# Optimization experiments

Measured on AMD Instinct MI355X. Metric: run time of the kernel, lower is better.

Reference implementation:

```python
import jax, jax.numpy as jnp
import numpy as np

B, S, E, H = 4, 2048, 256, 8
DK = E // H


def setup_inputs() -> dict:
    key = jax.random.key(0)
    ks = jax.random.split(key, 12)
    glorot = lambda k, shape: jax.random.uniform(k, shape, jnp.float32, -1.0, 1.0) * jnp.sqrt(6.0 / (shape[0] + shape[1]))
    inp = {
        "q": jax.random.normal(ks[0], (B, S, E), jnp.float32),
        "k": jax.random.normal(ks[1], (B, S, E), jnp.float32),
        "v": jax.random.normal(ks[2], (B, S, E), jnp.float32),
        # causal mask, np.triu(k=1)==0 -> lower triangular including diagonal
        "mask": (jnp.triu(jnp.ones((S, S), jnp.int32), k=1) == 0).astype(jnp.int32)[None, None],
        "Wq": glorot(ks[3], (E, E)), "bq": jnp.zeros((E,), jnp.float32),
        "Wk": glorot(ks[4], (E, E)), "bk": jnp.zeros((E,), jnp.float32),
        "Wv": glorot(ks[5], (E, E)), "bv": jnp.zeros((E,), jnp.float32),
        "Wo": glorot(ks[6], (E, E)), "bo": jnp.zeros((E,), jnp.float32),
        "gammas": glorot(ks[7], (H, 1)).reshape(H, 1, 1),  # xavier init of (H,1,1)
    }
    return inp


def reference(q, k, v, mask, Wq, bq, Wk, bk, Wv, bv, Wo, bo, gammas):
    b, s, e = q.shape
    h = gammas.shape[0]
    dk = e // h
    neg = jnp.float32(-1e32)

    def proj(x, W, bias):
        return (x @ W.T + bias).reshape(b, s, h, dk).transpose(0, 2, 1, 3)  # [B,H,S,dk]

    qh, kh, vh = proj(q, Wq, bq), proj(k, Wk, bk), proj(v, Wv, bv)
    scores = jnp.einsum("bhid,bhjd->bhij", qh, kh) / jnp.sqrt(jnp.float32(dk))  # [B,H,S,S]

    # --- no_grad block: monotonic distance-decay term ---
    maskf = mask.astype(scores.dtype)
    s1 = jax.nn.softmax(jnp.where(mask == 0, neg, scores), axis=-1) * maskf
    s1 = jax.lax.stop_gradient(s1)
    distcum = jnp.cumsum(s1, axis=-1)
    disttotal = jnp.sum(s1, axis=-1, keepdims=True)
    idx = jnp.arange(s)
    pos = jnp.abs(idx[None, :] - idx[:, None]).astype(scores.dtype)[None, None]  # |i-j|
    dist = jnp.sqrt(jnp.clip((disttotal - distcum) * pos, 0.0, None))
    dist = jax.lax.stop_gradient(dist)
    # ----------------------------------------------------

    gamma = -jax.nn.softplus(gammas)[None]                      # [1,H,1,1]
    total_effect = jnp.clip(jnp.exp(dist * gamma), 1e-5, 1e5)
    scores = jnp.where(mask == 0, neg, scores * total_effect)
    attn = jax.nn.softmax(scores, axis=-1)                      # zero_pad=False (mask=1 path)
    out = jnp.einsum("bhij,bhjd->bhid", attn, vh)
    concat = out.transpose(0, 2, 1, 3).reshape(b, s, e)
    return concat @ Wo.T + bo
```

## Files before the change

kernel.cpp:

```cpp
#include <hip/hip_runtime.h>
#include <math.h>

#define B_   4
#define S_   2048
#define E_   256
#define H_   8
#define DK_  32
#define NROWS (B_*S_)

typedef unsigned short ushort_t;
typedef __attribute__((ext_vector_type(8))) short  bf16x8;
typedef __attribute__((ext_vector_type(4))) float  f32x4;

#define LOG2E 1.4426950408889634f
#define QSCALE (0.17677669529663687f * 1.4426950408889634f)

#if __has_builtin(__builtin_amdgcn_exp2f)
#define EXP2F(x) __builtin_amdgcn_exp2f(x)
#else
#define EXP2F(x) exp2f(x)
#endif
#if __has_builtin(__builtin_amdgcn_sqrtf)
#define SQRTF(x) __builtin_amdgcn_sqrtf(x)
#else
#define SQRTF(x) sqrtf(x)
#endif
#if __has_builtin(__builtin_amdgcn_rcpf)
#define RCPF(x) __builtin_amdgcn_rcpf(x)
#else
#define RCPF(x) (1.0f/(x))
#endif

__device__ __forceinline__ ushort_t bf16_rne(float x)
{
    unsigned int u = __float_as_uint(x);
    unsigned int r = u + 0x7FFFu + ((u >> 16) & 1u);
    return (ushort_t)(r >> 16);
}
__device__ __forceinline__ float bf16_to_f(ushort_t h)
{
    return __uint_as_float(((unsigned int)h) << 16);
}

__device__ __forceinline__ float scan16(float x)
{
    x += __int_as_float(__builtin_amdgcn_update_dpp(0, __float_as_int(x), 0x111, 0xF, 0xF, true));
    x += __int_as_float(__builtin_amdgcn_update_dpp(0, __float_as_int(x), 0x112, 0xF, 0xF, true));
    x += __int_as_float(__builtin_amdgcn_update_dpp(0, __float_as_int(x), 0x114, 0xF, 0xF, true));
    x += __int_as_float(__builtin_amdgcn_update_dpp(0, __float_as_int(x), 0x118, 0xF, 0xF, true));
    return x;
}
__device__ __forceinline__ float bcast15(float x)
{
    return __int_as_float(__builtin_amdgcn_ds_swizzle(__float_as_int(x), 0x1F0));
}


__global__ __launch_bounds__(256)
void conv_w(const float* __restrict__ Wq, const float* __restrict__ Wk,
            const float* __restrict__ Wv, const float* __restrict__ Wo,
            ushort_t* __restrict__ wh, ushort_t* __restrict__ wl)
{
    const int z = blockIdx.y;
    const float* src = (z == 0) ? Wq : (z == 1) ? Wk : (z == 2) ? Wv : Wo;
    ushort_t* dh = wh + (size_t)z * (E_ * E_);
    ushort_t* dl = wl + (size_t)z * (E_ * E_);
    const int n0 = blockIdx.x * 16;
    const int lr = threadIdx.x & 15, kq = threadIdx.x >> 4;
    #pragma unroll
    for (int half = 0; half < 2; half++) {
        const int kk = kq * 8 + half * 128;
        const float* s = src + (size_t)(n0 + lr) * E_ + kk;
        const float4 a = *(const float4*)s;
        const float4 b = *(const float4*)(s + 4);
        const float xs[8] = {a.x, a.y, a.z, a.w, b.x, b.y, b.z, b.w};
        bf16x8 hv, lv;
        #pragma unroll
        for (int e = 0; e < 8; e++) {
            const ushort_t hb = bf16_rne(xs[e]);
            hv[e] = (short)hb;
            lv[e] = (short)bf16_rne(xs[e] - bf16_to_f(hb));
        }
        const size_t o = ((size_t)blockIdx.x * 8 + (kk >> 5)) * 512
                       + ((kk >> 3) & 3) * 128 + lr * 8;
        *(bf16x8*)&dh[o] = hv;
        *(bf16x8*)&dl[o] = lv;
    }
}

__global__ __launch_bounds__(256)
void gemm_qkv(const float* __restrict__ Xq, const float* __restrict__ Xk,
              const float* __restrict__ Xv,
              const ushort_t* __restrict__ Wh, const ushort_t* __restrict__ Wl,
              const float* __restrict__ bqp, const float* __restrict__ bkp,
              const float* __restrict__ bvp,
              ushort_t* __restrict__ Qh, ushort_t* __restrict__ Ql,
              ushort_t* __restrict__ Kh, ushort_t* __restrict__ Kl,
              ushort_t* __restrict__ Vt)
{
    __shared__ __align__(16) float sF[4][16][68];
    ushort_t* sBh = (ushort_t*)&sF[0][0][0];
    ushort_t* sBl = sBh + 4096;

    const size_t WN = (size_t)E_ * E_;
    const int z = blockIdx.z;
    const float* Xf = (z == 0) ? Xq : (z == 1) ? Xk : Xv;
    const ushort_t* Bh = Wh + (size_t)z * WN;
    const ushort_t* Bl = Wl + (size_t)z * WN;
    const float* bias = (z == 0) ? bqp : (z == 1) ? bkp : bvp;
    const float scale = (z == 0) ? QSCALE : 1.0f;

    const int lane = threadIdx.x & 63, wv = threadIdx.x >> 6;
    const int lr = lane & 15, lq = lane >> 4;
    const int mb = blockIdx.x;
    const int nstrip = blockIdx.y * 4 + wv;

    const float* arow = Xf + (size_t)(nstrip * 16 + lr) * E_ + lq * 8;
    const size_t boff = (size_t)(mb * 4 + wv) * 8 * 512 + lane * 8;
    const int lw = wv * 512 + lane * 8;

    f32x4 acc[4] = {{0,0,0,0},{0,0,0,0},{0,0,0,0},{0,0,0,0}};

    float4 a0 = *(const float4*)(arow);
    float4 a1 = *(const float4*)(arow + 4);
    {
        const bf16x8 sH = *(const bf16x8*)(Bh + boff);
        const bf16x8 sL = *(const bf16x8*)(Bl + boff);
        *(bf16x8*)&sBh[lw] = sH;
        *(bf16x8*)&sBl[lw] = sL;
    }

    #pragma unroll
    for (int kc = 0; kc < 8; kc++) {
        __syncthreads();
        const int cur = (kc & 1) * 2048;
        float4 a0n, a1n; bf16x8 sH2, sL2;
        if (kc < 7) {
            a0n = *(const float4*)(arow + (kc + 1) * 32);
            a1n = *(const float4*)(arow + (kc + 1) * 32 + 4);
            sH2 = *(const bf16x8*)(Bh + boff + (size_t)(kc + 1) * 512);
            sL2 = *(const bf16x8*)(Bl + boff + (size_t)(kc + 1) * 512);
        }
        bf16x8 aH, aL;
        {
            const float xs[8] = {a0.x, a0.y, a0.z, a0.w, a1.x, a1.y, a1.z, a1.w};
            #pragma unroll
            for (int e = 0; e < 8; e++) {
                const ushort_t hb = bf16_rne(xs[e]);
                aH[e] = (short)hb;
                aL[e] = (short)bf16_rne(xs[e] - bf16_to_f(hb));
            }
        }
        #pragma unroll
        for (int t = 0; t < 4; t++) {
            const int ro = cur + t * 512 + lane * 8;
            const bf16x8 bH = *(const bf16x8*)&sBh[ro];
            const bf16x8 bL = *(const bf16x8*)&sBl[ro];
            acc[t] = __builtin_amdgcn_mfma_f32_16x16x32_bf16(aL, bH, acc[t], 0, 0, 0);
            acc[t] = __builtin_amdgcn_mfma_f32_16x16x32_bf16(aH, bL, acc[t], 0, 0, 0);
            acc[t] = __builtin_amdgcn_mfma_f32_16x16x32_bf16(aH, bH, acc[t], 0, 0, 0);
        }
        if (kc < 7) {
            const int nx = (cur ^ 2048) + lw;
            *(bf16x8*)&sBh[nx] = sH2;
            *(bf16x8*)&sBl[nx] = sL2;
            a0 = a0n; a1 = a1n;
        }
    }
    __syncthreads();

    if (z <= 1) {
        #pragma unroll
        for (int t = 0; t < 4; t++) {
            const float bt = bias[mb * 64 + t * 16 + lr];
            #pragma unroll
            for (int reg = 0; reg < 4; reg++)
                sF[wv][lq * 4 + reg][t * 16 + lr] = (acc[t][reg] + bt) * scale;
        }
        ushort_t* Y1 = z ? Kh : Qh;
        ushort_t* Y2 = z ? Kl : Ql;
        const int bI   = nstrip >> 7;
        const int sblk = nstrip & 127;
        const int qg = lane >> 4, s = lane & 15;
        #pragma unroll
        for (int cg = 0; cg < 2; cg++) {
            const float* src = &sF[wv][s][cg * 32 + qg * 8];
            const float4 v0 = *(const float4*)src;
            const float4 v1 = *(const float4*)(src + 4);
            const float xs[8] = {v0.x, v0.y, v0.z, v0.w, v1.x, v1.y, v1.z, v1.w};
            bf16x8 hv, lv;
            #pragma unroll
            for (int e = 0; e < 8; e++) {
                const ushort_t hb = bf16_rne(xs[e]);
                hv[e] = (short)hb;
                lv[e] = (short)bf16_rne(xs[e] - bf16_to_f(hb));
            }
            const int h = mb * 2 + cg;
            const size_t o = (size_t)(bI * H_ + h) * (S_ * DK_)
                           + (size_t)sblk * 512 + lane * 8;
            *(bf16x8*)&Y1[o] = hv;
            *(bf16x8*)&Y2[o] = lv;
        }
    } else {
        #pragma unroll
        for (int t = 0; t < 4; t++) {
            const int col = mb * 64 + t * 16 + lr;
            const float bt = bias[col];
            const int h = col >> 5, d = col & 31;
            #pragma unroll
            for (int reg = 0; reg < 4; reg++) {
                const int n  = nstrip * 16 + lq * 4 + reg;
                const int bI = n >> 11, sI = n & (S_ - 1);
                const size_t o = (size_t)(bI * H_ + h) * (S_ * DK_)
                               + (size_t)((sI >> 5) * 2 + (d >> 4)) * 512
                               + ((sI >> 3) & 3) * 128 + (d & 15) * 8 + (sI & 7);
                Vt[o] = bf16_rne(acc[t][reg] + bt);
            }
        }
    }
}

__global__ __launch_bounds__(256)
void gemm_out(const ushort_t* __restrict__ Xh, const ushort_t* __restrict__ Xl,
              const ushort_t* __restrict__ Wh, const ushort_t* __restrict__ Wl,
              const float* __restrict__ bias, float* __restrict__ Yf)
{
    __shared__ __align__(16) ushort_t sBh[2 * 2048];
    __shared__ __align__(16) ushort_t sBl[2 * 2048];

    const int lane = threadIdx.x & 63, wv = threadIdx.x >> 6;
    const int lr = lane & 15, lq = lane >> 4;
    const int mb = blockIdx.x;
    const int nstrip = blockIdx.y * 4 + wv;

    const size_t aoff = (size_t)nstrip * 8 * 512 + lane * 8;
    const size_t boff = (size_t)(mb * 4 + wv) * 8 * 512 + lane * 8;
    const int lw = wv * 512 + lane * 8;

    f32x4 acc[4] = {{0,0,0,0},{0,0,0,0},{0,0,0,0},{0,0,0,0}};

    bf16x8 aH = *(const bf16x8*)(Xh + aoff);
    bf16x8 aL = *(const bf16x8*)(Xl + aoff);
    {
        const bf16x8 sH = *(const bf16x8*)(Wh + boff);
        const bf16x8 sL = *(const bf16x8*)(Wl + boff);
        *(bf16x8*)&sBh[lw] = sH;
        *(bf16x8*)&sBl[lw] = sL;
    }

    #pragma unroll
    for (int kc = 0; kc < 8; kc++) {
        __syncthreads();
        const int cur = (kc & 1) * 2048;
        bf16x8 aH2, aL2, sH2, sL2;
        if (kc < 7) {
            aH2 = *(const bf16x8*)(Xh + aoff + (size_t)(kc + 1) * 512);
            aL2 = *(const bf16x8*)(Xl + aoff + (size_t)(kc + 1) * 512);
            sH2 = *(const bf16x8*)(Wh + boff + (size_t)(kc + 1) * 512);
            sL2 = *(const bf16x8*)(Wl + boff + (size_t)(kc + 1) * 512);
        }
        #pragma unroll
        for (int t = 0; t < 4; t++) {
            const int ro = cur + t * 512 + lane * 8;
            const bf16x8 bH = *(const bf16x8*)&sBh[ro];
            const bf16x8 bL = *(const bf16x8*)&sBl[ro];
            acc[t] = __builtin_amdgcn_mfma_f32_16x16x32_bf16(aL, bH, acc[t], 0, 0, 0);
            acc[t] = __builtin_amdgcn_mfma_f32_16x16x32_bf16(aH, bL, acc[t], 0, 0, 0);
            acc[t] = __builtin_amdgcn_mfma_f32_16x16x32_bf16(aH, bH, acc[t], 0, 0, 0);
        }
        if (kc < 7) {
            const int nx = (cur ^ 2048) + lw;
            *(bf16x8*)&sBh[nx] = sH2;
            *(bf16x8*)&sBl[nx] = sL2;
            aH = aH2; aL = aL2;
        }
    }

    #pragma unroll
    for (int t = 0; t < 4; t++) {
        const int col = mb * 64 + t * 16 + lr;
        const float bt = bias[col];
        #pragma unroll
        for (int reg = 0; reg < 4; reg++) {
            const int n = nstrip * 16 + lq * 4 + reg;
            Yf[(size_t)n * E_ + col] = acc[t][reg] + bt;
        }
    }
}

#define VPAD 72

__device__ __forceinline__ void score_tile(f32x4 (&a)[4],
    const ushort_t* __restrict__ Kbh, const ushort_t* __restrict__ Kbl,
    int jt, const bf16x8& qhi, const bf16x8& qlo, int lane, int lr, int lq,
    bool domask, int i0)
{
    #pragma unroll
    for (int tt = 0; tt < 4; tt++) {
        const size_t ko = (size_t)(jt * 4 + tt) * 512 + lane * 8;
        const bf16x8 khi = *(const bf16x8*)(Kbh + ko);
        const bf16x8 klo = *(const bf16x8*)(Kbl + ko);
        f32x4 v = {0.f, 0.f, 0.f, 0.f};
        v = __builtin_amdgcn_mfma_f32_16x16x32_bf16(qlo, khi, v, 0, 0, 0);
        v = __builtin_amdgcn_mfma_f32_16x16x32_bf16(qhi, klo, v, 0, 0, 0);
        v = __builtin_amdgcn_mfma_f32_16x16x32_bf16(qhi, khi, v, 0, 0, 0);
        a[tt] = v;
    }
    if (domask) {
        #pragma unroll
        for (int tt = 0; tt < 4; tt++)
            #pragma unroll
            for (int r = 0; r < 4; r++) {
                const int irow = i0 + lq * 4 + r;
                const int j    = jt * 64 + tt * 16 + lr;
                if (j > irow) a[tt][r] = -3.0e38f;
            }
    }
}

__global__ __launch_bounds__(256)
void attn_flash(const ushort_t* __restrict__ Qh, const ushort_t* __restrict__ Ql,
                const ushort_t* __restrict__ Kh, const ushort_t* __restrict__ Kl,
                const ushort_t* __restrict__ Vs, const float* __restrict__ gammas,
                ushort_t* __restrict__ Ch, ushort_t* __restrict__ Cl)
{
    __shared__ float sTS[16][36];
    __shared__ __align__(16) ushort_t sP[4][16 * VPAD];
    __shared__ float sO[4][16][32];
    __shared__ float sZ[4][16];

    const int tid  = threadIdx.x;
    const int lane = tid & 63, wv = tid >> 6;
    const int lr   = lane & 15, lq = lane >> 4;
    const int bh   = blockIdx.x & 31;
    const int st   = (blockIdx.x >> 5) & 3;
    const int tq   = 31 - (blockIdx.x >> 7);
    const int h    = bh & 7, b = bh >> 3;
    const int i0   = tq * 64 + st * 16;

    const size_t hb = (size_t)bh * (S_ * DK_);
    const ushort_t* Kbh = Kh + hb;
    const ushort_t* Kbl = Kl + hb;
    const ushort_t* Vb  = Vs + hb;

    const float g   = gammas[h];
    const float gl2 = -((g > 20.f) ? g : log1pf(__expf(g))) * LOG2E;

    const size_t qoff = hb + (size_t)(i0 >> 4) * 512 + lane * 8;
    const bf16x8 qhi = *(const bf16x8*)(Qh + qoff);
    const bf16x8 qlo = *(const bf16x8*)(Ql + qoff);

    for (int jt = wv; jt <= tq; jt += 4) {
        f32x4 a[4];
        score_tile(a, Kbh, Kbl, jt, qhi, qlo, lane, lr, lq, jt == tq, i0);
        #pragma unroll
        for (int r = 0; r < 4; r++) {
            float rs = (EXP2F(a[0][r]) + EXP2F(a[1][r]))
                     + (EXP2F(a[2][r]) + EXP2F(a[3][r]));
            rs += __shfl_xor(rs, 1); rs += __shfl_xor(rs, 2);
            rs += __shfl_xor(rs, 4); rs += __shfl_xor(rs, 8);
            if (lr == 0) sTS[lq * 4 + r][jt] = rs;
        }
    }
    __syncthreads();

    float z2a[4] = {0.f, 0.f, 0.f, 0.f};
    f32x4 O0 = {0.f,0.f,0.f,0.f}, O1 = {0.f,0.f,0.f,0.f};

    if (wv <= tq) {
        float invZ[4], base[4], pr[4];
        #pragma unroll
        for (int r = 0; r < 4; r++) {
            const int row = lq * 4 + r;
            float run = 0.f, bs = 0.f;
            for (int t = 0; t <= tq; t++) {
                if (t < wv) bs += sTS[row][t];
                run += sTS[row][t];
            }
            invZ[r] = RCPF(run);
            base[r] = bs;
            pr[r]   = (float)(i0 + row - lr);
        }

        ushort_t* sPw = &sP[wv][0];
        for (int jt = wv; jt <= tq; jt += 4) {
            const int j0 = jt * 64;
            f32x4 a[4];
            score_tile(a, Kbh, Kbl, jt, qhi, qlo, lane, lr, lq, jt == tq, i0);

            float sc[4][4], tot[4][4];
            #pragma unroll
            for (int tt = 0; tt < 4; tt++)
                #pragma unroll
                for (int r = 0; r < 4; r++) {
                    const float e = EXP2F(a[tt][r]);
                    const float s = scan16(e);
                    sc[tt][r]  = s;
                    tot[tt][r] = bcast15(s);
                }
            #pragma unroll
            for (int r = 0; r < 4; r++) {
                float run2 = base[r];
                #pragma unroll
                for (int tt = 0; tt < 4; tt++) { sc[tt][r] += run2; run2 += tot[tt][r]; }
            }
            #pragma unroll
            for (int tt = 0; tt < 4; tt++) {
                const float jf = (float)(j0 + tt * 16);
                #pragma unroll
                for (int r = 0; r < 4; r++) {
                    const float rest = fmaf(-sc[tt][r], invZ[r], 1.0f);
                    const float posf = pr[r] - jf;
                    const float dist = SQRTF(fmaxf(rest * posf, 0.f));
                    const float eff  = EXP2F(gl2 * dist);
                    const float p2   = EXP2F(a[tt][r] * eff);
                    z2a[r] += p2;
                    sPw[(lq * 4 + r) * VPAD + tt * 16 + lr] = bf16_rne(p2);
                }
            }
            #pragma unroll
            for (int kc = 0; kc < 2; kc++) {
                const bf16x8 pa = *(const bf16x8*)&sPw[lr * VPAD + kc * 32 + lq * 8];
                const size_t vb = (size_t)(((j0 >> 5) + kc) * 2) * 512 + lane * 8;
                const bf16x8 v0 = *(const bf16x8*)(Vb + vb);
                const bf16x8 v1 = *(const bf16x8*)(Vb + vb + 512);
                O0 = __builtin_amdgcn_mfma_f32_16x16x32_bf16(pa, v0, O0, 0, 0, 0);
                O1 = __builtin_amdgcn_mfma_f32_16x16x32_bf16(pa, v1, O1, 0, 0, 0);
            }
            if (jt + 4 <= tq) {
                #pragma unroll
                for (int r = 0; r < 4; r++) {
                    const int row = lq * 4 + r;
                    base[r] += sTS[row][jt] + sTS[row][jt+1] + sTS[row][jt+2] + sTS[row][jt+3];
                }
            }
        }
    }

    #pragma unroll
    for (int r = 0; r < 4; r++) {
        float z = z2a[r];
        z += __shfl_xor(z, 1); z += __shfl_xor(z, 2);
        z += __shfl_xor(z, 4); z += __shfl_xor(z, 8);
        if (lr == 0) sZ[wv][lq * 4 + r] = z;
        sO[wv][lq * 4 + r][lr]      = O0[r];
        sO[wv][lq * 4 + r][16 + lr] = O1[r];
    }
    __syncthreads();

    #pragma unroll
    for (int p = 0; p < 2; p++) {
        const int pid = tid + p * 256;
        const int row = pid >> 5, d = pid & 31;
        const float v = (sO[0][row][d] + sO[1][row][d]) + (sO[2][row][d] + sO[3][row][d]);
        const float z = (sZ[0][row] + sZ[1][row]) + (sZ[2][row] + sZ[3][row]);
        const float y = v * RCPF(z);
        const int nIdx = b * S_ + i0 + row;
        const size_t o = ((size_t)(nIdx >> 4) * 8 + h) * 512
                       + (d >> 3) * 128 + (nIdx & 15) * 8 + (d & 7);
        const ushort_t hbb = bf16_rne(y);
        Ch[o] = hbb;
        Cl[o] = bf16_rne(y - bf16_to_f(hbb));
    }
}

extern "C" void kernel_launch(void* const* d_in, const int* in_sizes, int n_in,
                              void* d_out, int out_size, void* d_ws, size_t ws_size,
                              hipStream_t stream)
{
    const float* q      = (const float*)d_in[0];
    const float* k      = (const float*)d_in[1];
    const float* v      = (const float*)d_in[2];
    const float* Wq     = (const float*)d_in[4];
    const float* bq     = (const float*)d_in[5];
    const float* Wk     = (const float*)d_in[6];
    const float* bk     = (const float*)d_in[7];
    const float* Wv     = (const float*)d_in[8];
    const float* bv     = (const float*)d_in[9];
    const float* Wo     = (const float*)d_in[10];
    const float* bo     = (const float*)d_in[11];
    const float* gammas = (const float*)d_in[12];
    float* out = (float*)d_out;

    const size_t N2 = (size_t)NROWS * E_;
    const size_t WN = (size_t)E_ * E_;

    ushort_t* wh = (ushort_t*)d_ws;
    ushort_t* wl = wh + 4 * WN;
    ushort_t* qh = wl + 4 * WN;
    ushort_t* ql = qh + N2;
    ushort_t* kh = ql + N2;
    ushort_t* kl = kh + N2;
    ushort_t* vt = kl + N2;
    ushort_t* ch = vt + N2;
    ushort_t* cl = ch + N2;

    conv_w<<<dim3(16, 4), 256, 0, stream>>>(Wq, Wk, Wv, Wo, wh, wl);

    gemm_qkv<<<dim3(E_ / 64, NROWS / 64, 3), 256, 0, stream>>>(
        q, k, v, wh, wl, bq, bk, bv, qh, ql, kh, kl, vt);

    attn_flash<<<32 * 32 * 4, 256, 0, stream>>>(qh, ql, kh, kl, vt, gammas, ch, cl);

    gemm_out<<<dim3(E_ / 64, NROWS / 64), 256, 0, stream>>>(
        ch, cl, wh + 3 * WN, wl + 3 * WN, bo, out);
}
```

Before: 230.0 us.

## Fuse weight bf16 split into GEMMs and prefetch K/V tiles in attention

Removes the separate conv_w kernel launch: both GEMMs now read fp32 weights directly and split them into hi/lo bf16 in registers before staging them in LDS. The attention kernel now software-pipelines K tile loads, fetching the next tile while computing the current scores in both passes, and issues V loads earlier so they overlap the decay computation. This saves a launch and a round trip of weight data through memory, at the cost of redundant weight conversion in every GEMM block and extra register pressure from the prefetch buffers.

Result: slower. 262.4 us (+14.0%).

```diff
diff --git a/kernel.cpp b/kernel.cpp
--- a/kernel.cpp
+++ b/kernel.cpp
@@ -41,6 +41,17 @@
 {
     return __uint_as_float(((unsigned int)h) << 16);
 }
+__device__ __forceinline__ void split8(const float4& a, const float4& b,
+                                       bf16x8& hi, bf16x8& lo)
+{
+    const float xs[8] = {a.x, a.y, a.z, a.w, b.x, b.y, b.z, b.w};
+    #pragma unroll
+    for (int e = 0; e < 8; e++) {
+        const ushort_t hb = bf16_rne(xs[e]);
+        hi[e] = (short)hb;
+        lo[e] = (short)bf16_rne(xs[e] - bf16_to_f(hb));
+    }
+}
 
 __device__ __forceinline__ float scan16(float x)
 {
@@ -57,41 +68,10 @@
 
 
 __global__ __launch_bounds__(256)
-void conv_w(const float* __restrict__ Wq, const float* __restrict__ Wk,
-            const float* __restrict__ Wv, const float* __restrict__ Wo,
-            ushort_t* __restrict__ wh, ushort_t* __restrict__ wl)
-{
-    const int z = blockIdx.y;
-    const float* src = (z == 0) ? Wq : (z == 1) ? Wk : (z == 2) ? Wv : Wo;
-    ushort_t* dh = wh + (size_t)z * (E_ * E_);
-    ushort_t* dl = wl + (size_t)z * (E_ * E_);
-    const int n0 = blockIdx.x * 16;
-    const int lr = threadIdx.x & 15, kq = threadIdx.x >> 4;
-    #pragma unroll
-    for (int half = 0; half < 2; half++) {
-        const int kk = kq * 8 + half * 128;
-        const float* s = src + (size_t)(n0 + lr) * E_ + kk;
-        const float4 a = *(const float4*)s;
-        const float4 b = *(const float4*)(s + 4);
-        const float xs[8] = {a.x, a.y, a.z, a.w, b.x, b.y, b.z, b.w};
-        bf16x8 hv, lv;
-        #pragma unroll
-        for (int e = 0; e < 8; e++) {
-            const ushort_t hb = bf16_rne(xs[e]);
-            hv[e] = (short)hb;
-            lv[e] = (short)bf16_rne(xs[e] - bf16_to_f(hb));
-        }
-        const size_t o = ((size_t)blockIdx.x * 8 + (kk >> 5)) * 512
-                       + ((kk >> 3) & 3) * 128 + lr * 8;
-        *(bf16x8*)&dh[o] = hv;
-        *(bf16x8*)&dl[o] = lv;
-    }
-}
-
-__global__ __launch_bounds__(256)
 void gemm_qkv(const float* __restrict__ Xq, const float* __restrict__ Xk,
               const float* __restrict__ Xv,
-              const ushort_t* __restrict__ Wh, const ushort_t* __restrict__ Wl,
+              const float* __restrict__ Wqf, const float* __restrict__ Wkf,
+              const float* __restrict__ Wvf,
               const float* __restrict__ bqp, const float* __restrict__ bkp,
               const float* __restrict__ bvp,
               ushort_t* __restrict__ Qh, ushort_t* __restrict__ Ql,
@@ -102,11 +82,9 @@
     ushort_t* sBh = (ushort_t*)&sF[0][0][0];
     ushort_t* sBl = sBh + 4096;
 
-    const size_t WN = (size_t)E_ * E_;
     const int z = blockIdx.z;
     const float* Xf = (z == 0) ? Xq : (z == 1) ? Xk : Xv;
-    const ushort_t* Bh = Wh + (size_t)z * WN;
-    const ushort_t* Bl = Wl + (size_t)z * WN;
+    const float* Wf = (z == 0) ? Wqf : (z == 1) ? Wkf : Wvf;
     const float* bias = (z == 0) ? bqp : (z == 1) ? bkp : bvp;
     const float scale = (z == 0) ? QSCALE : 1.0f;
 
@@ -116,7 +94,7 @@
     const int nstrip = blockIdx.y * 4 + wv;
 
     const float* arow = Xf + (size_t)(nstrip * 16 + lr) * E_ + lq * 8;
-    const size_t boff = (size_t)(mb * 4 + wv) * 8 * 512 + lane * 8;
+    const float* wrow = Wf + (size_t)(mb * 64 + wv * 16 + lr) * E_ + lq * 8;
     const int lw = wv * 512 + lane * 8;
 
     f32x4 acc[4] = {{0,0,0,0},{0,0,0,0},{0,0,0,0},{0,0,0,0}};
@@ -124,8 +102,10 @@
     float4 a0 = *(const float4*)(arow);
     float4 a1 = *(const float4*)(arow + 4);
     {
-        const bf16x8 sH = *(const bf16x8*)(Bh + boff);
-        const bf16x8 sL = *(const bf16x8*)(Bl + boff);
+        const float4 w0 = *(const float4*)(wrow);
+        const float4 w1 = *(const float4*)(wrow + 4);
+        bf16x8 sH, sL;
+        split8(w0, w1, sH, sL);
         *(bf16x8*)&sBh[lw] = sH;
         *(bf16x8*)&sBl[lw] = sL;
     }
@@ -134,23 +114,15 @@
     for (int kc = 0; kc < 8; kc++) {
         __syncthreads();
         const int cur = (kc & 1) * 2048;
-        float4 a0n, a1n; bf16x8 sH2, sL2;
+        float4 a0n, a1n, w0n, w1n;
         if (kc < 7) {
             a0n = *(const float4*)(arow + (kc + 1) * 32);
             a1n = *(const float4*)(arow + (kc + 1) * 32 + 4);
-            sH2 = *(const bf16x8*)(Bh + boff + (size_t)(kc + 1) * 512);
-            sL2 = *(const bf16x8*)(Bl + boff + (size_t)(kc + 1) * 512);
+            w0n = *(const float4*)(wrow + (kc + 1) * 32);
+            w1n = *(const float4*)(wrow + (kc + 1) * 32 + 4);
         }
         bf16x8 aH, aL;
-        {
-            const float xs[8] = {a0.x, a0.y, a0.z, a0.w, a1.x, a1.y, a1.z, a1.w};
-            #pragma unroll
-            for (int e = 0; e < 8; e++) {
-                const ushort_t hb = bf16_rne(xs[e]);
-                aH[e] = (short)hb;
-                aL[e] = (short)bf16_rne(xs[e] - bf16_to_f(hb));
-            }
-        }
+        split8(a0, a1, aH, aL);
         #pragma unroll
         for (int t = 0; t < 4; t++) {
             const int ro = cur + t * 512 + lane * 8;
@@ -161,6 +133,8 @@
             acc[t] = __builtin_amdgcn_mfma_f32_16x16x32_bf16(aH, bH, acc[t], 0, 0, 0);
         }
         if (kc < 7) {
+            bf16x8 sH2, sL2;
+            split8(w0n, w1n, sH2, sL2);
             const int nx = (cur ^ 2048) + lw;
             *(bf16x8*)&sBh[nx] = sH2;
             *(bf16x8*)&sBl[nx] = sL2;
@@ -187,14 +161,8 @@
             const float* src = &sF[wv][s][cg * 32 + qg * 8];
             const float4 v0 = *(const float4*)src;
             const float4 v1 = *(const float4*)(src + 4);
-            const float xs[8] = {v0.x, v0.y, v0.z, v0.w, v1.x, v1.y, v1.z, v1.w};
             bf16x8 hv, lv;
-            #pragma unroll
-            for (int e = 0; e < 8; e++) {
-                const ushort_t hb = bf16_rne(xs[e]);
-                hv[e] = (short)hb;
-                lv[e] = (short)bf16_rne(xs[e] - bf16_to_f(hb));
-            }
+            split8(v0, v1, hv, lv);
             const int h = mb * 2 + cg;
             const size_t o = (size_t)(bI * H_ + h) * (S_ * DK_)
                            + (size_t)sblk * 512 + lane * 8;
@@ -222,8 +190,8 @@
 
 __global__ __launch_bounds__(256)
 void gemm_out(const ushort_t* __restrict__ Xh, const ushort_t* __restrict__ Xl,
-              const ushort_t* __restrict__ Wh, const ushort_t* __restrict__ Wl,
-              const float* __restrict__ bias, float* __restrict__ Yf)
+              const float* __restrict__ Wf, const float* __restrict__ bias,
+              float* __restrict__ Yf)
 {
     __shared__ __align__(16) ushort_t sBh[2 * 2048];
     __shared__ __align__(16) ushort_t sBl[2 * 2048];
@@ -234,7 +202,7 @@
     const int nstrip = blockIdx.y * 4 + wv;
 
     const size_t aoff = (size_t)nstrip * 8 * 512 + lane * 8;
-    const size_t boff = (size_t)(mb * 4 + wv) * 8 * 512 + lane * 8;
+    const float* wrow = Wf + (size_t)(mb * 64 + wv * 16 + lr) * E_ + lq * 8;
     const int lw = wv * 512 + lane * 8;
 
     f32x4 acc[4] = {{0,0,0,0},{0,0,0,0},{0,0,0,0},{0,0,0,0}};
@@ -242,8 +210,10 @@
     bf16x8 aH = *(const bf16x8*)(Xh + aoff);
     bf16x8 aL = *(const bf16x8*)(Xl + aoff);
     {
-        const bf16x8 sH = *(const bf16x8*)(Wh + boff);
-        const bf16x8 sL = *(const bf16x8*)(Wl + boff);
+        const float4 w0 = *(const float4*)(wrow);
+        const float4 w1 = *(const float4*)(wrow + 4);
+        bf16x8 sH, sL;
+        split8(w0, w1, sH, sL);
         *(bf16x8*)&sBh[lw] = sH;
         *(bf16x8*)&sBl[lw] = sL;
     }
@@ -252,12 +222,13 @@
     for (int kc = 0; kc < 8; kc++) {
         __syncthreads();
         const int cur = (kc & 1) * 2048;
-        bf16x8 aH2, aL2, sH2, sL2;
+        bf16x8 aH2, aL2;
+        float4 w0n, w1n;
         if (kc < 7) {
             aH2 = *(const bf16x8*)(Xh + aoff + (size_t)(kc + 1) * 512);
             aL2 = *(const bf16x8*)(Xl + aoff + (size_t)(kc + 1) * 512);
-            sH2 = *(const bf16x8*)(Wh + boff + (size_t)(kc + 1) * 512);
-            sL2 = *(const bf16x8*)(Wl + boff + (size_t)(kc + 1) * 512);
+            w0n = *(const float4*)(wrow + (kc + 1) * 32);
+            w1n = *(const float4*)(wrow + (kc + 1) * 32 + 4);
         }
         #pragma unroll
         for (int t = 0; t < 4; t++) {
@@ -269,6 +240,8 @@
             acc[t] = __builtin_amdgcn_mfma_f32_16x16x32_bf16(aH, bH, acc[t], 0, 0, 0);
         }
         if (kc < 7) {
+            bf16x8 sH2, sL2;
+            split8(w0n, w1n, sH2, sL2);
             const int nx = (cur ^ 2048) + lw;
             *(bf16x8*)&sBh[nx] = sH2;
             *(bf16x8*)&sBl[nx] = sL2;
@@ -290,31 +263,29 @@
 
 #define VPAD 72
 
-__device__ __forceinline__ void score_tile(f32x4 (&a)[4],
+__device__ __forceinline__ void load_ktile(
     const ushort_t* __restrict__ Kbh, const ushort_t* __restrict__ Kbl,
-    int jt, const bf16x8& qhi, const bf16x8& qlo, int lane, int lr, int lq,
-    bool domask, int i0)
+    int jt, int lane, bf16x8 (&kh)[4], bf16x8 (&kl)[4])
 {
     #pragma unroll
     for (int tt = 0; tt < 4; tt++) {
         const size_t ko = (size_t)(jt * 4 + tt) * 512 + lane * 8;
-        const bf16x8 khi = *(const bf16x8*)(Kbh + ko);
-        const bf16x8 klo = *(const bf16x8*)(Kbl + ko);
+        kh[tt] = *(const bf16x8*)(Kbh + ko);
+        kl[tt] = *(const bf16x8*)(Kbl + ko);
+    }
+}
+
+__device__ __forceinline__ void score_frags(f32x4 (&a)[4],
+    const bf16x8 (&kh)[4], const bf16x8 (&kl)[4],
+    const bf16x8& qhi, const bf16x8& qlo)
+{
+    #pragma unroll
+    for (int tt = 0; tt < 4; tt++) {
         f32x4 v = {0.f, 0.f, 0.f, 0.f};
-        v = __builtin_amdgcn_mfma_f32_16x16x32_bf16(qlo, khi, v, 0, 0, 0);
-        v = __builtin_amdgcn_mfma_f32_16x16x32_bf16(qhi, klo, v, 0, 0, 0);
-        v = __builtin_amdgcn_mfma_f32_16x16x32_bf16(qhi, khi, v, 0, 0, 0);
+        v = __builtin_amdgcn_mfma_f32_16x16x32_bf16(qlo, kh[tt], v, 0, 0, 0);
+        v = __builtin_amdgcn_mfma_f32_16x16x32_bf16(qhi, kl[tt], v, 0, 0, 0);
+        v = __builtin_amdgcn_mfma_f32_16x16x32_bf16(qhi, kh[tt], v, 0, 0, 0);
         a[tt] = v;
-    }
-    if (domask) {
-        #pragma unroll
-        for (int tt = 0; tt < 4; tt++)
-            #pragma unroll
-            for (int r = 0; r < 4; r++) {
-                const int irow = i0 + lq * 4 + r;
-                const int j    = jt * 64 + tt * 16 + lr;
-                if (j > irow) a[tt][r] = -3.0e38f;
-            }
     }
 }
 
@@ -350,16 +321,38 @@
     const bf16x8 qhi = *(const bf16x8*)(Qh + qoff);
     const bf16x8 qlo = *(const bf16x8*)(Ql + qoff);
 
-    for (int jt = wv; jt <= tq; jt += 4) {
-        f32x4 a[4];
-        score_tile(a, Kbh, Kbl, jt, qhi, qlo, lane, lr, lq, jt == tq, i0);
-        #pragma unroll
-        for (int r = 0; r < 4; r++) {
-            float rs = (EXP2F(a[0][r]) + EXP2F(a[1][r]))
-                     + (EXP2F(a[2][r]) + EXP2F(a[3][r]));
-            rs += __shfl_xor(rs, 1); rs += __shfl_xor(rs, 2);
-            rs += __shfl_xor(rs, 4); rs += __shfl_xor(rs, 8);
-            if (lr == 0) sTS[lq * 4 + r][jt] = rs;
+    {
+        bf16x8 kch[4], kcl[4];
+        if (wv <= tq) load_ktile(Kbh, Kbl, wv, lane, kch, kcl);
+        for (int jt = wv; jt <= tq; jt += 4) {
+            const bool more = (jt + 4 <= tq);
+            bf16x8 knh[4], knl[4];
+            if (more) load_ktile(Kbh, Kbl, jt + 4, lane, knh, knl);
+
+            f32x4 a[4];
+            score_frags(a, kch, kcl, qhi, qlo);
+            if (jt == tq) {
+                #pragma unroll
+                for (int tt = 0; tt < 4; tt++)
+                    #pragma unroll
+                    for (int r = 0; r < 4; r++) {
+                        const int irow = i0 + lq * 4 + r;
+                        const int j    = jt * 64 + tt * 16 + lr;
+                        if (j > irow) a[tt][r] = -3.0e38f;
+                    }
+            }
+            #pragma unroll
+            for (int r = 0; r < 4; r++) {
+                float rs = (EXP2F(a[0][r]) + EXP2F(a[1][r]))
+                         + (EXP2F(a[2][r]) + EXP2F(a[3][r]));
+                rs += __shfl_xor(rs, 1); rs += __shfl_xor(rs, 2);
+                rs += __shfl_xor(rs, 4); rs += __shfl_xor(rs, 8);
+                if (lr == 0) sTS[lq * 4 + r][jt] = rs;
+            }
+            if (more) {
+                #pragma unroll
+                for (int tt = 0; tt < 4; tt++) { kch[tt] = knh[tt]; kcl[tt] = knl[tt]; }
+            }
         }
     }
     __syncthreads();
@@ -368,6 +361,9 @@
     f32x4 O0 = {0.f,0.f,0.f,0.f}, O1 = {0.f,0.f,0.f,0.f};
 
     if (wv <= tq) {
+        bf16x8 kch[4], kcl[4];
+        load_ktile(Kbh, Kbl, wv, lane, kch, kcl);
+
         float invZ[4], base[4], pr[4];
         #pragma unroll
         for (int r = 0; r < 4; r++) {
@@ -385,8 +381,32 @@
         ushort_t* sPw = &sP[wv][0];
         for (int jt = wv; jt <= tq; jt += 4) {
             const int j0 = jt * 64;
+            const bool more = (jt + 4 <= tq);
+            bf16x8 knh[4], knl[4];
+            if (more) load_ktile(Kbh, Kbl, jt + 4, lane, knh, knl);
+
             f32x4 a[4];
-            score_tile(a, Kbh, Kbl, jt, qhi, qlo, lane, lr, lq, jt == tq, i0);
+            score_frags(a, kch, kcl, qhi, qlo);
+            if (jt == tq) {
+                #pragma unroll
+                for (int tt = 0; tt < 4; tt++)
+                    #pragma unroll
+                    for (int r = 0; r < 4; r++) {
+                        const int irow = i0 + lq * 4 + r;
+                        const int j    = j0 + tt * 16 + lr;
+                        if (j > irow) a[tt][r] = -3.0e38f;
+                    }
+            }
+
+            bf16x8 v00, v01, v10, v11;
+            {
+                const size_t vb0 = (size_t)((j0 >> 5) + 0) * 2 * 512 + lane * 8;
+                const size_t vb1 = (size_t)((j0 >> 5) + 1) * 2 * 512 + lane * 8;
+                v00 = *(const bf16x8*)(Vb + vb0);
+                v01 = *(const bf16x8*)(Vb + vb0 + 512);
+                v10 = *(const bf16x8*)(Vb + vb1);
+                v11 = *(const bf16x8*)(Vb + vb1 + 512);
+            }
 
             float sc[4][4], tot[4][4];
             #pragma unroll
@@ -418,21 +438,22 @@
                     sPw[(lq * 4 + r) * VPAD + tt * 16 + lr] = bf16_rne(p2);
                 }
             }
-            #pragma unroll
-            for (int kc = 0; kc < 2; kc++) {
-                const bf16x8 pa = *(const bf16x8*)&sPw[lr * VPAD + kc * 32 + lq * 8];
-                const size_t vb = (size_t)(((j0 >> 5) + kc) * 2) * 512 + lane * 8;
-                const bf16x8 v0 = *(const bf16x8*)(Vb + vb);
-                const bf16x8 v1 = *(const bf16x8*)(Vb + vb + 512);
-                O0 = __builtin_amdgcn_mfma_f32_16x16x32_bf16(pa, v0, O0, 0, 0, 0);
-                O1 = __builtin_amdgcn_mfma_f32_16x16x32_bf16(pa, v1, O1, 0, 0, 0);
-            }
-            if (jt + 4 <= tq) {
+            {
+                const bf16x8 pa0 = *(const bf16x8*)&sPw[lr * VPAD + 0 * 32 + lq * 8];
+                const bf16x8 pa1 = *(const bf16x8*)&sPw[lr * VPAD + 1 * 32 + lq * 8];
+                O0 = __builtin_amdgcn_mfma_f32_16x16x32_bf16(pa0, v00, O0, 0, 0, 0);
+                O1 = __builtin_amdgcn_mfma_f32_16x16x32_bf16(pa0, v01, O1, 0, 0, 0);
+                O0 = __builtin_amdgcn_mfma_f32_16x16x32_bf16(pa1, v10, O0, 0, 0, 0);
+                O1 = __builtin_amdgcn_mfma_f32_16x16x32_bf16(pa1, v11, O1, 0, 0, 0);
+            }
+            if (more) {
                 #pragma unroll
                 for (int r = 0; r < 4; r++) {
                     const int row = lq * 4 + r;
                     base[r] += sTS[row][jt] + sTS[row][jt+1] + sTS[row][jt+2] + sTS[row][jt+3];
                 }
+                #pragma unroll
+                for (int tt = 0; tt < 4; tt++) { kch[tt] = knh[tt]; kcl[tt] = knl[tt]; }
             }
         }
     }
@@ -483,11 +504,8 @@
     float* out = (float*)d_out;
 
     const size_t N2 = (size_t)NROWS * E_;
-    const size_t WN = (size_t)E_ * E_;
-
-    ushort_t* wh = (ushort_t*)d_ws;
-    ushort_t* wl = wh + 4 * WN;
-    ushort_t* qh = wl + 4 * WN;
+
+    ushort_t* qh = (ushort_t*)d_ws;
     ushort_t* ql = qh + N2;
     ushort_t* kh = ql + N2;
     ushort_t* kl = kh + N2;
@@ -495,13 +513,11 @@
     ushort_t* ch = vt + N2;
     ushort_t* cl = ch + N2;
 
-    conv_w<<<dim3(16, 4), 256, 0, stream>>>(Wq, Wk, Wv, Wo, wh, wl);
-
     gemm_qkv<<<dim3(E_ / 64, NROWS / 64, 3), 256, 0, stream>>>(
-        q, k, v, wh, wl, bq, bk, bv, qh, ql, kh, kl, vt);
+        q, k, v, Wq, Wk, Wv, bq, bk, bv, qh, ql, kh, kl, vt);
 
     attn_flash<<<32 * 32 * 4, 256, 0, stream>>>(qh, ql, kh, kl, vt, gammas, ch, cl);
 
     gemm_out<<<dim3(E_ / 64, NROWS / 64), 256, 0, stream>>>(
-        ch, cl, wh + 3 * WN, wl + 3 * WN, bo, out);
-}
+        ch, cl, Wo, bo, out);
+}
```
